# Optimization experiments

Measured on AMD Instinct MI355X. Metric: run time of the kernel, lower is better.

The kernel has to match this reference:

```python
import jax, jax.numpy as jnp
import numpy as np

N, F, E, G = 100000, 128, 600000, 1000
EPS = 1e-5


def setup_inputs() -> dict:
    key = jax.random.key(0)
    k1, k2, k3, k4 = jax.random.split(key, 4)
    x = jax.random.normal(k1, (N, F), dtype=jnp.float32)
    graph_id = jnp.sort(jax.random.randint(k2, (N,), 0, G, dtype=jnp.int32))
    edge_src = jax.random.randint(k3, (E,), 0, N, dtype=jnp.int32)
    edge_dst = jax.random.randint(k4, (E,), 0, N, dtype=jnp.int32)
    return {
        "x": x,
        "gamma": jnp.ones((F,), jnp.float32),
        "beta": jnp.zeros((F,), jnp.float32),
        "lambda_batch": jnp.ones((F,), jnp.float32),
        "lambda_graph": jnp.ones((F,), jnp.float32),
        "lambda_adja": jnp.ones((F,), jnp.float32),
        "lambda_node": jnp.ones((F,), jnp.float32),
        "graph_id": graph_id,
        "edge_src": edge_src,
        "edge_dst": edge_dst,
    }


def _batch_norm(x):
    # BatchNorm1d in training mode: biased stats over the node (batch) axis.
    mu = jnp.mean(x, axis=0, keepdims=True)
    var = jnp.mean(jnp.square(x), axis=0, keepdims=True) - jnp.square(mu)
    return (x - mu) * jax.lax.rsqrt(var + EPS)


def _graph_norm(x, graph_id):
    # Per-graph mean/var per feature via segment reductions. graph_id: [N]
    ones = jnp.ones((x.shape[0],), x.dtype)
    cnt = jax.ops.segment_sum(ones, graph_id, num_segments=G)  # [G]
    cnt = jnp.maximum(cnt, 1.0)[:, None]
    s = jax.ops.segment_sum(x, graph_id, num_segments=G)               # [G,F]
    s2 = jax.ops.segment_sum(jnp.square(x), graph_id, num_segments=G)  # [G,F]
    mu = s / cnt
    var = jnp.maximum(s2 / cnt - jnp.square(mu), 0.0)
    return (x - mu[graph_id]) * jax.lax.rsqrt(var[graph_id] + EPS)


def _adja_node_norm(x, edge_src, edge_dst):
    # Per-node stats over in-neighbors: normalize x_i with mean/var of {x_j : j->i}.
    msg = x[edge_src]  # [E,F]
    deg = jax.ops.segment_sum(jnp.ones((E,), x.dtype), edge_dst, num_segments=N)
    deg = jnp.maximum(deg, 1.0)[:, None]
    s = jax.ops.segment_sum(msg, edge_dst, num_segments=N)
    s2 = jax.ops.segment_sum(jnp.square(msg), edge_dst, num_segments=N)
    mu = s / deg
    var = jnp.maximum(s2 / deg - jnp.square(mu), 0.0)
    return (x - mu) * jax.lax.rsqrt(var + EPS)


def _node_norm(x):
    # LayerNorm over feature axis, no affine.
    mu = jnp.mean(x, axis=-1, keepdims=True)
    var = jnp.mean(jnp.square(x - mu), axis=-1, keepdims=True)
    return (x - mu) * jax.lax.rsqrt(var + EPS)


def reference(x, gamma, beta, lambda_batch, lambda_graph, lambda_adja,
              lambda_node, graph_id, edge_src, edge_dst):
    x_b = _batch_norm(x)
    x_g = _graph_norm(x, graph_id)
    x_a = _adja_node_norm(x, edge_src, edge_dst)
    x_n = _node_norm(x)
    # norm_lambda(): softmax across the four lambda vectors per feature.
    lam = jax.nn.softmax(jnp.stack([lambda_batch, lambda_graph, lambda_adja,
                                    lambda_node], axis=0), axis=0)  # [4,F]
    x_new = lam[0] * x_b + lam[1] * x_g + lam[2] * x_a + lam[3] * x_n
    return gamma * x_new + beta
```

## Files before the change

### kernel.cpp

```cpp
#include <hip/hip_runtime.h>

#define N_NODES 100000
#define NF      128
#define NE      600000
#define NG      1000
#define EPSF    1e-5f

#define SCHUNK  1024
#define SCAN_NB ((N_NODES + SCHUNK - 1) / SCHUNK)

__global__ void k_deg(const int* __restrict__ dst, int* __restrict__ deg) {
    int e = blockIdx.x * 256 + threadIdx.x;
    if (e < NE) atomicAdd(&deg[dst[e]], 1);
}

__global__ __launch_bounds__(256) void k_stats(
    const float* __restrict__ x, const int* __restrict__ gid,
    float* __restrict__ gsum, float* __restrict__ gsq, int* __restrict__ cnt)
{
    const int wave = threadIdx.x >> 6;
    const int lane = threadIdx.x & 63;
    const int f = lane * 2;
    const int r0 = blockIdx.x * 32 + wave * 8;
    const int r1 = r0 + 8;

    float gsx = 0.f, gsy = 0.f, gqx = 0.f, gqy = 0.f;
    int cur = gid[r0];
    int runStart = r0;

    for (int r = r0; r < r1; ++r) {
        int g = gid[r];
        if (g != cur) {
            atomicAdd(&gsum[cur * NF + f],     gsx);
            atomicAdd(&gsum[cur * NF + f + 1], gsy);
            atomicAdd(&gsq [cur * NF + f],     gqx);
            atomicAdd(&gsq [cur * NF + f + 1], gqy);
            if (lane == 0) atomicAdd(&cnt[cur], r - runStart);
            gsx = gsy = gqx = gqy = 0.f;
            cur = g; runStart = r;
        }
        const float2 v = *reinterpret_cast<const float2*>(x + (size_t)r * NF + f);
        gsx += v.x; gsy += v.y; gqx += v.x * v.x; gqy += v.y * v.y;
    }
    atomicAdd(&gsum[cur * NF + f],     gsx);
    atomicAdd(&gsum[cur * NF + f + 1], gsy);
    atomicAdd(&gsq [cur * NF + f],     gqx);
    atomicAdd(&gsq [cur * NF + f + 1], gqy);
    if (lane == 0) atomicAdd(&cnt[cur], r1 - runStart);
}

__global__ __launch_bounds__(256) void k_bred(
    const float* __restrict__ gsum, const float* __restrict__ gsq,
    float* __restrict__ bsum, float* __restrict__ bsq)
{
    int t = threadIdx.x, b = blockIdx.x;
    int f = t & 127, gl = t >> 7;
    float s = 0.f, q = 0.f;
#pragma unroll
    for (int k = 0; k < 8; ++k) {
        int g = b * 16 + gl * 8 + k;
        if (g < NG) { s += gsum[g * NF + f]; q += gsq[g * NF + f]; }
    }
    atomicAdd(&bsum[f], s);
    atomicAdd(&bsq[f], q);
}

__global__ void k_scan1(const int* __restrict__ deg, int* __restrict__ bsums) {
    __shared__ int sdata[256];
    int b = blockIdx.x, t = threadIdx.x;
    int base = b * SCHUNK;
    int s = 0;
#pragma unroll
    for (int k = 0; k < 4; ++k) {
        int i = base + t * 4 + k;
        if (i < N_NODES) s += deg[i];
    }
    sdata[t] = s; __syncthreads();
    for (int st = 128; st > 0; st >>= 1) {
        if (t < st) sdata[t] += sdata[t + st];
        __syncthreads();
    }
    if (t == 0) bsums[b] = sdata[0];
}

__global__ void k_scan2(int* __restrict__ bsums) {
    if (threadIdx.x == 0 && blockIdx.x == 0) {
        int acc = 0;
        for (int i = 0; i < SCAN_NB; ++i) { int v = bsums[i]; bsums[i] = acc; acc += v; }
    }
}

__global__ void k_scan3(const int* __restrict__ deg, const int* __restrict__ bsums,
                        int* __restrict__ off) {
    __shared__ int sdata[256];
    int b = blockIdx.x, t = threadIdx.x;
    int base = b * SCHUNK;
    int loc[4]; int s = 0;
#pragma unroll
    for (int k = 0; k < 4; ++k) {
        int i = base + t * 4 + k;
        loc[k] = (i < N_NODES) ? deg[i] : 0;
        s += loc[k];
    }
    sdata[t] = s; __syncthreads();
    for (int st = 1; st < 256; st <<= 1) {
        int v = (t >= st) ? sdata[t - st] : 0;
        __syncthreads();
        sdata[t] += v;
        __syncthreads();
    }
    int run = bsums[b] + (sdata[t] - s);
#pragma unroll
    for (int k = 0; k < 4; ++k) {
        int i = base + t * 4 + k;
        if (i < N_NODES) { off[i] = run; run += loc[k]; }
    }
    if (b == 0 && t == 0) off[N_NODES] = NE;
}

__global__ void k_fill(const int* __restrict__ src, const int* __restrict__ dst,
                       const int* __restrict__ off, int* __restrict__ cursor,
                       int* __restrict__ nbr) {
    int e = blockIdx.x * 256 + threadIdx.x;
    if (e < NE) {
        int d = dst[e];
        int p = atomicAdd(&cursor[d], 1);
        nbr[off[d] + p] = src[e];
    }
}

__global__ __launch_bounds__(256) void k_prep(
    float* __restrict__ gsum, float* __restrict__ gsq, const int* __restrict__ cnt,
    const float* __restrict__ bsum, const float* __restrict__ bsq,
    const float* __restrict__ gamma, const float* __restrict__ beta,
    const float* __restrict__ lb, const float* __restrict__ lg,
    const float* __restrict__ la, const float* __restrict__ ln,
    float* __restrict__ fc)
{
    int b = blockIdx.x;
    if (b < (NG * NF) / 256) {
        int idx = b * 256 + threadIdx.x;
        int g = idx >> 7;
        float c = (float)cnt[g]; if (c < 1.f) c = 1.f;
        float rc = 1.0f / c;
        float m = gsum[idx] * rc;
        float v = gsq[idx] * rc - m * m; if (v < 0.f) v = 0.f;
        gsum[idx] = m;
        gsq[idx]  = rsqrtf(v + EPSF);
    } else if (threadIdx.x < NF) {
        int f = threadIdx.x;
        float mb = bsum[f] * (1.0f / N_NODES);
        float vb = bsq[f] * (1.0f / N_NODES) - mb * mb;
        float rvb = rsqrtf(vb + EPSF);
        float l0 = lb[f], l1 = lg[f], l2 = la[f], l3 = ln[f];
        float m = fmaxf(fmaxf(l0, l1), fmaxf(l2, l3));
        float w0 = __expf(l0 - m), w1 = __expf(l1 - m), w2 = __expf(l2 - m), w3 = __expf(l3 - m);
        float rs = gamma[f] / (w0 + w1 + w2 + w3);
        float* p = fc + f * 8;
        p[0] = mb; p[1] = rvb;
        p[2] = w0 * rs; p[3] = w1 * rs; p[4] = w2 * rs; p[5] = w3 * rs;
        p[6] = beta[f]; p[7] = 0.f;
    }
}

__global__ __launch_bounds__(256) void k_final(
    const float* __restrict__ x, const int* __restrict__ gid,
    const float* __restrict__ gmu, const float* __restrict__ grs,
    const float* __restrict__ fc,
    const int* __restrict__ off, const int* __restrict__ nbr,
    float* __restrict__ out)
{
    const int wave = threadIdx.x >> 6;
    const int lane = threadIdx.x & 63;
    const int i = blockIdx.x * 4 + wave;
    const int f = lane * 2;

    const float2 xi = *reinterpret_cast<const float2*>(x + (size_t)i * NF + f);

    const float4 c0 = *reinterpret_cast<const float4*>(fc + f * 8);
    const float4 c1 = *reinterpret_cast<const float4*>(fc + f * 8 + 4);
    const float4 d0 = *reinterpret_cast<const float4*>(fc + (f + 1) * 8);
    const float4 d1 = *reinterpret_cast<const float4*>(fc + (f + 1) * 8 + 4);

    float xbx = (xi.x - c0.x) * c0.y;
    float xby = (xi.y - d0.x) * d0.y;

    const int g = gid[i];
    const float2 mg = *reinterpret_cast<const float2*>(gmu + (size_t)g * NF + f);
    const float2 rg = *reinterpret_cast<const float2*>(grs + (size_t)g * NF + f);
    float xgx = (xi.x - mg.x) * rg.x;
    float xgy = (xi.y - mg.y) * rg.y;

    float s = xi.x + xi.y;
#pragma unroll
    for (int d = 1; d < 64; d <<= 1) s += __shfl_xor(s, d, 64);
    const float mn = s * (1.0f / NF);
    float dxx = xi.x - mn, dyy = xi.y - mn;
    float q = dxx * dxx + dyy * dyy;
#pragma unroll
    for (int d = 1; d < 64; d <<= 1) q += __shfl_xor(q, d, 64);
    const float rvn = rsqrtf(q * (1.0f / NF) + EPSF);
    float xnx = dxx * rvn, xny = dyy * rvn;

    const int e0 = off[i], e1 = off[i + 1];
    float asx = 0.f, asy = 0.f, aqx = 0.f, aqy = 0.f;
    int e = e0;
    for (; e + 4 <= e1; e += 4) {
        int j0 = nbr[e], j1 = nbr[e + 1], j2 = nbr[e + 2], j3 = nbr[e + 3];
        const float2 v0 = *reinterpret_cast<const float2*>(x + (size_t)j0 * NF + f);
        const float2 v1 = *reinterpret_cast<const float2*>(x + (size_t)j1 * NF + f);
        const float2 v2 = *reinterpret_cast<const float2*>(x + (size_t)j2 * NF + f);
        const float2 v3 = *reinterpret_cast<const float2*>(x + (size_t)j3 * NF + f);
        asx += v0.x; asy += v0.y; aqx += v0.x * v0.x; aqy += v0.y * v0.y;
        asx += v1.x; asy += v1.y; aqx += v1.x * v1.x; aqy += v1.y * v1.y;
        asx += v2.x; asy += v2.y; aqx += v2.x * v2.x; aqy += v2.y * v2.y;
        asx += v3.x; asy += v3.y; aqx += v3.x * v3.x; aqy += v3.y * v3.y;
    }
    for (; e < e1; ++e) {
        int j = nbr[e];
        const float2 v = *reinterpret_cast<const float2*>(x + (size_t)j * NF + f);
        asx += v.x; asy += v.y; aqx += v.x * v.x; aqy += v.y * v.y;
    }
    float dgc = (float)(e1 - e0); if (dgc < 1.f) dgc = 1.f;
    float rdg = 1.0f / dgc;
    float max_ = asx * rdg, may_ = asy * rdg;
    float vax = aqx * rdg - max_ * max_; if (vax < 0.f) vax = 0.f;
    float vay = aqy * rdg - may_ * may_; if (vay < 0.f) vay = 0.f;
    float xax = (xi.x - max_) * rsqrtf(vax + EPSF);
    float xay = (xi.y - may_) * rsqrtf(vay + EPSF);

    float outx = c0.z * xbx + c0.w * xgx + c1.x * xax + c1.y * xnx + c1.z;
    float outy = d0.z * xby + d0.w * xgy + d1.x * xay + d1.y * xny + d1.z;
    *reinterpret_cast<float2*>(out + (size_t)i * NF + f) = make_float2(outx, outy);
}

extern "C" void kernel_launch(void* const* d_in, const int* in_sizes, int n_in,
                              void* d_out, int out_size, void* d_ws, size_t ws_size,
                              hipStream_t stream) {
    const float* x     = (const float*)d_in[0];
    const float* gamma = (const float*)d_in[1];
    const float* beta  = (const float*)d_in[2];
    const float* lb    = (const float*)d_in[3];
    const float* lg    = (const float*)d_in[4];
    const float* la    = (const float*)d_in[5];
    const float* ln    = (const float*)d_in[6];
    const int*   gid   = (const int*)d_in[7];
    const int*   esrc  = (const int*)d_in[8];
    const int*   edst  = (const int*)d_in[9];
    float*       out   = (float*)d_out;

    float* ws    = (float*)d_ws;
    float* bsum  = ws;
    float* bsq   = bsum + NF;
    float* gsum  = bsq + NF;
    float* gsq   = gsum + (size_t)NG * NF;
    int*   cnt   = (int*)(gsq + (size_t)NG * NF);
    int*   deg   = cnt + NG;
    int*   cursor= deg + N_NODES;
    int*   off   = cursor + N_NODES;
    int*   bsums = off + (N_NODES + 1);
    int*   nbr   = bsums + 512;
    float* fc    = (float*)(nbr + NE);

    size_t zero_elems = (size_t)2 * NF + (size_t)2 * NG * NF + NG + (size_t)2 * N_NODES;
    hipMemsetAsync(d_ws, 0, zero_elems * sizeof(float), stream);

    k_deg  <<<(NE + 255) / 256, 256, 0, stream>>>(edst, deg);
    k_stats<<<N_NODES / 32, 256, 0, stream>>>(x, gid, gsum, gsq, cnt);
    k_bred <<<64, 256, 0, stream>>>(gsum, gsq, bsum, bsq);
    k_scan1<<<SCAN_NB, 256, 0, stream>>>(deg, bsums);
    k_scan2<<<1, 64, 0, stream>>>(bsums);
    k_scan3<<<SCAN_NB, 256, 0, stream>>>(deg, bsums, off);
    k_fill <<<(NE + 255) / 256, 256, 0, stream>>>(esrc, edst, off, cursor, nbr);
    k_prep <<<(NG * NF) / 256 + 1, 256, 0, stream>>>(gsum, gsq, cnt, bsum, bsq,
                                                     gamma, beta, lb, lg, la, ln, fc);
    k_final<<<N_NODES / 4, 256, 0, stream>>>(x, gid, gsum, gsq, fc, off, nbr, out);
}
```

Baseline: 275.6 us.

## Fuse preprocessing into three kernels with atomic wave-scan allocation and dual-node gather

Merges the degree count with the graph stats kernel, swaps the three-pass global prefix scan for a wave-level shuffle scan whose base offsets come from an atomic counter (the CSR is no longer ordered by node, only contiguous per node), and merges the CSR fill with the parameter prep. The final kernel now handles two nodes per wave, loading eight neighbour indices per node with masking so that more gathers are in flight. This cuts the launch count from nine to four and raises memory-level parallelism, at the cost of more registers and some wasted masked loads for low-degree nodes. A hidden ordering risk: k2's bred blocks read gsum while k1 has finished, which is fine, but k3's prep reads bsum written by k2, which kernel order on the same stream guarantees.

```diff
diff --git a/kernel.cpp b/kernel.cpp
--- a/kernel.cpp
+++ b/kernel.cpp
@@ -6,18 +6,29 @@
 #define NG      1000
 #define EPSF    1e-5f
 
-#define SCHUNK  1024
-#define SCAN_NB ((N_NODES + SCHUNK - 1) / SCHUNK)
-
-__global__ void k_deg(const int* __restrict__ dst, int* __restrict__ deg) {
-    int e = blockIdx.x * 256 + threadIdx.x;
-    if (e < NE) atomicAdd(&deg[dst[e]], 1);
-}
-
-__global__ __launch_bounds__(256) void k_stats(
+#define STATS_NB (N_NODES / 32)
+#define DEG_NB   (((NE / 4) + 255) / 256)
+#define ALLOC_NB ((N_NODES + 255) / 256)
+#define BRED_NB  64
+#define PREP_NB  ((NG * NF) / 256 + 1)
+
+__global__ __launch_bounds__(256) void k1_stats_deg(
     const float* __restrict__ x, const int* __restrict__ gid,
-    float* __restrict__ gsum, float* __restrict__ gsq, int* __restrict__ cnt)
-{
+    const int* __restrict__ edst,
+    float* __restrict__ gsum, float* __restrict__ gsq, int* __restrict__ cnt,
+    int* __restrict__ deg)
+{
+    if (blockIdx.x >= STATS_NB) {
+        int t = (blockIdx.x - STATS_NB) * 256 + threadIdx.x;
+        if (t < NE / 4) {
+            const int4 d4 = reinterpret_cast<const int4*>(edst)[t];
+            atomicAdd(&deg[d4.x], 1);
+            atomicAdd(&deg[d4.y], 1);
+            atomicAdd(&deg[d4.z], 1);
+            atomicAdd(&deg[d4.w], 1);
+        }
+        return;
+    }
     const int wave = threadIdx.x >> 6;
     const int lane = threadIdx.x & 63;
     const int f = lane * 2;
@@ -49,87 +60,49 @@
     if (lane == 0) atomicAdd(&cnt[cur], r1 - runStart);
 }
 
-__global__ __launch_bounds__(256) void k_bred(
+__global__ __launch_bounds__(256) void k2_alloc_bred(
+    const int* __restrict__ deg, int2* __restrict__ odeg, int* __restrict__ cursor,
+    int* __restrict__ total,
     const float* __restrict__ gsum, const float* __restrict__ gsq,
     float* __restrict__ bsum, float* __restrict__ bsq)
 {
-    int t = threadIdx.x, b = blockIdx.x;
-    int f = t & 127, gl = t >> 7;
-    float s = 0.f, q = 0.f;
-#pragma unroll
-    for (int k = 0; k < 8; ++k) {
-        int g = b * 16 + gl * 8 + k;
-        if (g < NG) { s += gsum[g * NF + f]; q += gsq[g * NF + f]; }
-    }
-    atomicAdd(&bsum[f], s);
-    atomicAdd(&bsq[f], q);
-}
-
-__global__ void k_scan1(const int* __restrict__ deg, int* __restrict__ bsums) {
-    __shared__ int sdata[256];
-    int b = blockIdx.x, t = threadIdx.x;
-    int base = b * SCHUNK;
-    int s = 0;
-#pragma unroll
-    for (int k = 0; k < 4; ++k) {
-        int i = base + t * 4 + k;
-        if (i < N_NODES) s += deg[i];
-    }
-    sdata[t] = s; __syncthreads();
-    for (int st = 128; st > 0; st >>= 1) {
-        if (t < st) sdata[t] += sdata[t + st];
-        __syncthreads();
-    }
-    if (t == 0) bsums[b] = sdata[0];
-}
-
-__global__ void k_scan2(int* __restrict__ bsums) {
-    if (threadIdx.x == 0 && blockIdx.x == 0) {
-        int acc = 0;
-        for (int i = 0; i < SCAN_NB; ++i) { int v = bsums[i]; bsums[i] = acc; acc += v; }
-    }
-}
-
-__global__ void k_scan3(const int* __restrict__ deg, const int* __restrict__ bsums,
-                        int* __restrict__ off) {
-    __shared__ int sdata[256];
-    int b = blockIdx.x, t = threadIdx.x;
-    int base = b * SCHUNK;
-    int loc[4]; int s = 0;
-#pragma unroll
-    for (int k = 0; k < 4; ++k) {
-        int i = base + t * 4 + k;
-        loc[k] = (i < N_NODES) ? deg[i] : 0;
-        s += loc[k];
-    }
-    sdata[t] = s; __syncthreads();
-    for (int st = 1; st < 256; st <<= 1) {
-        int v = (t >= st) ? sdata[t - st] : 0;
-        __syncthreads();
-        sdata[t] += v;
-        __syncthreads();
-    }
-    int run = bsums[b] + (sdata[t] - s);
-#pragma unroll
-    for (int k = 0; k < 4; ++k) {
-        int i = base + t * 4 + k;
-        if (i < N_NODES) { off[i] = run; run += loc[k]; }
-    }
-    if (b == 0 && t == 0) off[N_NODES] = NE;
-}
-
-__global__ void k_fill(const int* __restrict__ src, const int* __restrict__ dst,
-                       const int* __restrict__ off, int* __restrict__ cursor,
-                       int* __restrict__ nbr) {
-    int e = blockIdx.x * 256 + threadIdx.x;
-    if (e < NE) {
-        int d = dst[e];
-        int p = atomicAdd(&cursor[d], 1);
-        nbr[off[d] + p] = src[e];
-    }
-}
-
-__global__ __launch_bounds__(256) void k_prep(
+    if (blockIdx.x < ALLOC_NB) {
+        const int i = blockIdx.x * 256 + threadIdx.x;
+        const int lane = threadIdx.x & 63;
+        int d = (i < N_NODES) ? deg[i] : 0;
+        int p = d;
+#pragma unroll
+        for (int st = 1; st < 64; st <<= 1) {
+            int v = __shfl_up(p, st, 64);
+            if (lane >= st) p += v;
+        }
+        int wtot = __shfl(p, 63, 64);
+        int base = 0;
+        if (lane == 63) base = atomicAdd(total, wtot);
+        base = __shfl(base, 63, 64);
+        if (i < N_NODES) {
+            int o = base + p - d;
+            odeg[i] = make_int2(o, d);
+            cursor[i] = o;
+        }
+    } else {
+        int b = blockIdx.x - ALLOC_NB;
+        int t = threadIdx.x;
+        int f = t & 127, gl = t >> 7;
+        float s = 0.f, q = 0.f;
+#pragma unroll
+        for (int k = 0; k < 8; ++k) {
+            int g = b * 16 + gl * 8 + k;
+            if (g < NG) { s += gsum[g * NF + f]; q += gsq[g * NF + f]; }
+        }
+        atomicAdd(&bsum[f], s);
+        atomicAdd(&bsq[f], q);
+    }
+}
+
+__global__ __launch_bounds__(256) void k3_fill_prep(
+    const int* __restrict__ esrc, const int* __restrict__ edst,
+    int* __restrict__ cursor, int* __restrict__ nbr,
     float* __restrict__ gsum, float* __restrict__ gsq, const int* __restrict__ cnt,
     const float* __restrict__ bsum, const float* __restrict__ bsq,
     const float* __restrict__ gamma, const float* __restrict__ beta,
@@ -137,7 +110,20 @@
     const float* __restrict__ la, const float* __restrict__ ln,
     float* __restrict__ fc)
 {
-    int b = blockIdx.x;
+    if (blockIdx.x < DEG_NB) {
+        int t = blockIdx.x * 256 + threadIdx.x;
+        if (t < NE / 4) {
+            const int4 d4 = reinterpret_cast<const int4*>(edst)[t];
+            const int4 s4 = reinterpret_cast<const int4*>(esrc)[t];
+            int p;
+            p = atomicAdd(&cursor[d4.x], 1); nbr[p] = s4.x;
+            p = atomicAdd(&cursor[d4.y], 1); nbr[p] = s4.y;
+            p = atomicAdd(&cursor[d4.z], 1); nbr[p] = s4.z;
+            p = atomicAdd(&cursor[d4.w], 1); nbr[p] = s4.w;
+        }
+        return;
+    }
+    int b = blockIdx.x - DEG_NB;
     if (b < (NG * NF) / 256) {
         int idx = b * 256 + threadIdx.x;
         int g = idx >> 7;
@@ -163,75 +149,109 @@
     }
 }
 
-__global__ __launch_bounds__(256) void k_final(
+__global__ __launch_bounds__(256) void k5_final(
     const float* __restrict__ x, const int* __restrict__ gid,
     const float* __restrict__ gmu, const float* __restrict__ grs,
-    const float* __restrict__ fc,
-    const int* __restrict__ off, const int* __restrict__ nbr,
-    float* __restrict__ out)
+    const float* __restrict__ fc, const int2* __restrict__ odeg,
+    const int* __restrict__ nbr, float* __restrict__ out)
 {
     const int wave = threadIdx.x >> 6;
     const int lane = threadIdx.x & 63;
-    const int i = blockIdx.x * 4 + wave;
+    const int i0 = blockIdx.x * 8 + wave * 2;
+    const int i1 = i0 + 1;
     const int f = lane * 2;
 
-    const float2 xi = *reinterpret_cast<const float2*>(x + (size_t)i * NF + f);
+    const float2 xa = *reinterpret_cast<const float2*>(x + (size_t)i0 * NF + f);
+    const float2 xb = *reinterpret_cast<const float2*>(x + (size_t)i1 * NF + f);
 
     const float4 c0 = *reinterpret_cast<const float4*>(fc + f * 8);
     const float4 c1 = *reinterpret_cast<const float4*>(fc + f * 8 + 4);
     const float4 d0 = *reinterpret_cast<const float4*>(fc + (f + 1) * 8);
     const float4 d1 = *reinterpret_cast<const float4*>(fc + (f + 1) * 8 + 4);
 
-    float xbx = (xi.x - c0.x) * c0.y;
-    float xby = (xi.y - d0.x) * d0.y;
-
-    const int g = gid[i];
-    const float2 mg = *reinterpret_cast<const float2*>(gmu + (size_t)g * NF + f);
-    const float2 rg = *reinterpret_cast<const float2*>(grs + (size_t)g * NF + f);
-    float xgx = (xi.x - mg.x) * rg.x;
-    float xgy = (xi.y - mg.y) * rg.y;
-
-    float s = xi.x + xi.y;
-#pragma unroll
-    for (int d = 1; d < 64; d <<= 1) s += __shfl_xor(s, d, 64);
-    const float mn = s * (1.0f / NF);
-    float dxx = xi.x - mn, dyy = xi.y - mn;
-    float q = dxx * dxx + dyy * dyy;
-#pragma unroll
-    for (int d = 1; d < 64; d <<= 1) q += __shfl_xor(q, d, 64);
-    const float rvn = rsqrtf(q * (1.0f / NF) + EPSF);
-    float xnx = dxx * rvn, xny = dyy * rvn;
-
-    const int e0 = off[i], e1 = off[i + 1];
+    const int2 oa = odeg[i0], ob = odeg[i1];
+    const int sa = oa.x, da = oa.y, sb = ob.x, db = ob.y;
     float asx = 0.f, asy = 0.f, aqx = 0.f, aqy = 0.f;
-    int e = e0;
-    for (; e + 4 <= e1; e += 4) {
-        int j0 = nbr[e], j1 = nbr[e + 1], j2 = nbr[e + 2], j3 = nbr[e + 3];
-        const float2 v0 = *reinterpret_cast<const float2*>(x + (size_t)j0 * NF + f);
-        const float2 v1 = *reinterpret_cast<const float2*>(x + (size_t)j1 * NF + f);
-        const float2 v2 = *reinterpret_cast<const float2*>(x + (size_t)j2 * NF + f);
-        const float2 v3 = *reinterpret_cast<const float2*>(x + (size_t)j3 * NF + f);
-        asx += v0.x; asy += v0.y; aqx += v0.x * v0.x; aqy += v0.y * v0.y;
-        asx += v1.x; asy += v1.y; aqx += v1.x * v1.x; aqy += v1.y * v1.y;
-        asx += v2.x; asy += v2.y; aqx += v2.x * v2.x; aqy += v2.y * v2.y;
-        asx += v3.x; asy += v3.y; aqx += v3.x * v3.x; aqy += v3.y * v3.y;
-    }
-    for (; e < e1; ++e) {
-        int j = nbr[e];
-        const float2 v = *reinterpret_cast<const float2*>(x + (size_t)j * NF + f);
-        asx += v.x; asy += v.y; aqx += v.x * v.x; aqy += v.y * v.y;
-    }
-    float dgc = (float)(e1 - e0); if (dgc < 1.f) dgc = 1.f;
-    float rdg = 1.0f / dgc;
-    float max_ = asx * rdg, may_ = asy * rdg;
-    float vax = aqx * rdg - max_ * max_; if (vax < 0.f) vax = 0.f;
-    float vay = aqy * rdg - may_ * may_; if (vay < 0.f) vay = 0.f;
-    float xax = (xi.x - max_) * rsqrtf(vax + EPSF);
-    float xay = (xi.y - may_) * rsqrtf(vay + EPSF);
-
-    float outx = c0.z * xbx + c0.w * xgx + c1.x * xax + c1.y * xnx + c1.z;
-    float outy = d0.z * xby + d0.w * xgy + d1.x * xay + d1.y * xny + d1.z;
-    *reinterpret_cast<float2*>(out + (size_t)i * NF + f) = make_float2(outx, outy);
+    float bsx = 0.f, bsy = 0.f, bqx = 0.f, bqy = 0.f;
+    int ka = 0, kb = 0;
+    while (ka < da || kb < db) {
+        int ia_[8], ib_[8];
+        const bool hA = ka < da, hB = kb < db;
+        if (hA) {
+#pragma unroll
+            for (int k = 0; k < 8; ++k)
+                ia_[k] = nbr[(ka + k < da) ? (sa + ka + k) : sa];
+        }
+        if (hB) {
+#pragma unroll
+            for (int k = 0; k < 8; ++k)
+                ib_[k] = nbr[(kb + k < db) ? (sb + kb + k) : sb];
+        }
+        if (hA) {
+#pragma unroll
+            for (int k = 0; k < 8; ++k) {
+                const float2 v = *reinterpret_cast<const float2*>(x + (size_t)ia_[k] * NF + f);
+                const float m = (ka + k < da) ? 1.f : 0.f;
+                asx += m * v.x; asy += m * v.y;
+                aqx += m * v.x * v.x; aqy += m * v.y * v.y;
+            }
+        }
+        if (hB) {
+#pragma unroll
+            for (int k = 0; k < 8; ++k) {
+                const float2 v = *reinterpret_cast<const float2*>(x + (size_t)ib_[k] * NF + f);
+                const float m = (kb + k < db) ? 1.f : 0.f;
+                bsx += m * v.x; bsy += m * v.y;
+                bqx += m * v.x * v.x; bqy += m * v.y * v.y;
+            }
+        }
+        ka += 8; kb += 8;
+    }
+
+    float xba_x = (xa.x - c0.x) * c0.y, xba_y = (xa.y - d0.x) * d0.y;
+    float xbb_x = (xb.x - c0.x) * c0.y, xbb_y = (xb.y - d0.x) * d0.y;
+
+    const int ga = gid[i0], gb = gid[i1];
+    const float2 mga = *reinterpret_cast<const float2*>(gmu + (size_t)ga * NF + f);
+    const float2 rga = *reinterpret_cast<const float2*>(grs + (size_t)ga * NF + f);
+    const float2 mgb = *reinterpret_cast<const float2*>(gmu + (size_t)gb * NF + f);
+    const float2 rgb = *reinterpret_cast<const float2*>(grs + (size_t)gb * NF + f);
+    float xga_x = (xa.x - mga.x) * rga.x, xga_y = (xa.y - mga.y) * rga.y;
+    float xgb_x = (xb.x - mgb.x) * rgb.x, xgb_y = (xb.y - mgb.y) * rgb.y;
+
+    float sA = xa.x + xa.y, sB = xb.x + xb.y;
+#pragma unroll
+    for (int d = 1; d < 64; d <<= 1) { sA += __shfl_xor(sA, d, 64); sB += __shfl_xor(sB, d, 64); }
+    const float mnA = sA * (1.0f / NF), mnB = sB * (1.0f / NF);
+    float dax = xa.x - mnA, day = xa.y - mnA, dbx = xb.x - mnB, dby = xb.y - mnB;
+    float qA = dax * dax + day * day, qB = dbx * dbx + dby * dby;
+#pragma unroll
+    for (int d = 1; d < 64; d <<= 1) { qA += __shfl_xor(qA, d, 64); qB += __shfl_xor(qB, d, 64); }
+    const float rvnA = rsqrtf(qA * (1.0f / NF) + EPSF);
+    const float rvnB = rsqrtf(qB * (1.0f / NF) + EPSF);
+    float xna_x = dax * rvnA, xna_y = day * rvnA;
+    float xnb_x = dbx * rvnB, xnb_y = dby * rvnB;
+
+    float dga = (float)da; if (dga < 1.f) dga = 1.f;
+    float dgb = (float)db; if (dgb < 1.f) dgb = 1.f;
+    float rda = 1.0f / dga, rdb = 1.0f / dgb;
+    float maa = asx * rda, mab = asy * rda;
+    float vaa = aqx * rda - maa * maa; if (vaa < 0.f) vaa = 0.f;
+    float vab = aqy * rda - mab * mab; if (vab < 0.f) vab = 0.f;
+    float xaa_x = (xa.x - maa) * rsqrtf(vaa + EPSF);
+    float xaa_y = (xa.y - mab) * rsqrtf(vab + EPSF);
+    float mba = bsx * rdb, mbb = bsy * rdb;
+    float vba = bqx * rdb - mba * mba; if (vba < 0.f) vba = 0.f;
+    float vbb = bqy * rdb - mbb * mbb; if (vbb < 0.f) vbb = 0.f;
+    float xab_x = (xb.x - mba) * rsqrtf(vba + EPSF);
+    float xab_y = (xb.y - mbb) * rsqrtf(vbb + EPSF);
+
+    float oa_x = c0.z * xba_x + c0.w * xga_x + c1.x * xaa_x + c1.y * xna_x + c1.z;
+    float oa_y = d0.z * xba_y + d0.w * xga_y + d1.x * xaa_y + d1.y * xna_y + d1.z;
+    float ob_x = c0.z * xbb_x + c0.w * xgb_x + c1.x * xab_x + c1.y * xnb_x + c1.z;
+    float ob_y = d0.z * xbb_y + d0.w * xgb_y + d1.x * xab_y + d1.y * xnb_y + d1.z;
+    *reinterpret_cast<float2*>(out + (size_t)i0 * NF + f) = make_float2(oa_x, oa_y);
+    *reinterpret_cast<float2*>(out + (size_t)i1 * NF + f) = make_float2(ob_x, ob_y);
 }
 
 extern "C" void kernel_launch(void* const* d_in, const int* in_sizes, int n_in,
@@ -256,23 +276,22 @@
     float* gsq   = gsum + (size_t)NG * NF;
     int*   cnt   = (int*)(gsq + (size_t)NG * NF);
     int*   deg   = cnt + NG;
-    int*   cursor= deg + N_NODES;
-    int*   off   = cursor + N_NODES;
-    int*   bsums = off + (N_NODES + 1);
-    int*   nbr   = bsums + 512;
+    int*   total = deg + N_NODES;
+    int*   cursor= total + 2;
+    int2*  odeg  = (int2*)(cursor + N_NODES);
+    int*   nbr   = (int*)(odeg + N_NODES);
     float* fc    = (float*)(nbr + NE);
 
-    size_t zero_elems = (size_t)2 * NF + (size_t)2 * NG * NF + NG + (size_t)2 * N_NODES;
+    const size_t zero_elems = (size_t)2 * NF + (size_t)2 * NG * NF + NG + N_NODES + 2;
     hipMemsetAsync(d_ws, 0, zero_elems * sizeof(float), stream);
 
-    k_deg  <<<(NE + 255) / 256, 256, 0, stream>>>(edst, deg);
-    k_stats<<<N_NODES / 32, 256, 0, stream>>>(x, gid, gsum, gsq, cnt);
-    k_bred <<<64, 256, 0, stream>>>(gsum, gsq, bsum, bsq);
-    k_scan1<<<SCAN_NB, 256, 0, stream>>>(deg, bsums);
-    k_scan2<<<1, 64, 0, stream>>>(bsums);
-    k_scan3<<<SCAN_NB, 256, 0, stream>>>(deg, bsums, off);
-    k_fill <<<(NE + 255) / 256, 256, 0, stream>>>(esrc, edst, off, cursor, nbr);
-    k_prep <<<(NG * NF) / 256 + 1, 256, 0, stream>>>(gsum, gsq, cnt, bsum, bsq,
-                                                     gamma, beta, lb, lg, la, ln, fc);
-    k_final<<<N_NODES / 4, 256, 0, stream>>>(x, gid, gsum, gsq, fc, off, nbr, out);
-}
+    k1_stats_deg<<<STATS_NB + DEG_NB, 256, 0, stream>>>(
+        x, gid, edst, gsum, gsq, cnt, deg);
+    k2_alloc_bred<<<ALLOC_NB + BRED_NB, 256, 0, stream>>>(
+        deg, odeg, cursor, total, gsum, gsq, bsum, bsq);
+    k3_fill_prep<<<DEG_NB + PREP_NB, 256, 0, stream>>>(
+        esrc, edst, cursor, nbr, gsum, gsq, cnt, bsum, bsq,
+        gamma, beta, lb, lg, la, ln, fc);
+    k5_final<<<N_NODES / 8, 256, 0, stream>>>(
+        x, gid, gsum, gsq, fc, odeg, nbr, out);
+}
```

Result: slower. 288.5 us (+4.7%).
